# Performance work log

Hardware: AMD Instinct MI355X
Metric: run time of the kernel (lower is better)

## Reference

```python
import jax, jax.numpy as jnp
import numpy as np

DIN, HID = 256, 512
SCALE = 1.0 / (64.0 * 6.0 ** 2)  # q / 2304, as in the torch code
NEG = 9e15


def setup_inputs() -> dict:
    key = jax.random.key(0)
    ks = jax.random.split(key, 8)
    B, N = 32, 1024
    x = jax.random.normal(ks[0], (B, N, DIN), dtype=jnp.float32)
    mask = jax.random.randint(ks[1], (B, N, N), 0, 2).astype(jnp.float32)
    lim = 1.0 / np.sqrt(DIN)
    Wv = jax.random.uniform(ks[2], (DIN, HID), minval=-lim, maxval=lim, dtype=jnp.float32)
    bv = jax.random.uniform(ks[3], (HID,), minval=-lim, maxval=lim, dtype=jnp.float32)
    Wk = jax.random.uniform(ks[4], (DIN, HID), minval=-lim, maxval=lim, dtype=jnp.float32)
    bk = jax.random.uniform(ks[5], (HID,), minval=-lim, maxval=lim, dtype=jnp.float32)
    Wq = jax.random.uniform(ks[6], (DIN, HID), minval=-lim, maxval=lim, dtype=jnp.float32)
    bq = jax.random.uniform(ks[7], (HID,), minval=-lim, maxval=lim, dtype=jnp.float32)
    return {"x": x, "mask": mask, "Wv": Wv, "bv": bv, "Wk": Wk, "bk": bk, "Wq": Wq, "bq": bq}


def reference(x, mask, Wv, bv, Wk, bk, Wq, bq):
    v = jax.nn.relu(x @ Wv + bv)                      # [B,N,H]
    q = jax.nn.relu(x @ Wq + bq)                      # [B,N,H]
    k = jax.nn.relu(x @ Wk + bk)                      # [B,N,H]
    scores = jnp.einsum('bnh,bmh->bnm', q * SCALE, k)  # [B,N,N]
    att = jax.nn.softmax(scores * mask - NEG * (1.0 - mask), axis=2)
    out = jax.nn.relu(jnp.einsum('bnm,bmh->bnh', att, v))
    return out
```

## Files before the change

kernel.cpp:

```cpp
#include <hip/hip_runtime.h>
#include <hip/hip_bf16.h>

#define DIN   256
#define HID   512
#define NBAT  32
#define NSEQ  1024
#define SCALEF (1.0f / 2304.0f)
#define NEGC  9e15f

typedef __attribute__((ext_vector_type(4))) float f32x4;
typedef __attribute__((ext_vector_type(8))) short bf16x8;
typedef unsigned short u16;

__device__ __forceinline__ u16 f2bf(float f) {
    union { float f; unsigned u; } v; v.f = f;
    unsigned r = v.u + 0x7fffu + ((v.u >> 16) & 1u);
    return (u16)(r >> 16);
}

__device__ __forceinline__ float bf2f(u16 b) {
    union { unsigned u; float f; } v; v.u = ((unsigned)b) << 16;
    return v.f;
}

__device__ __forceinline__ void g2lds16(const void* g, void* l) {
    __builtin_amdgcn_global_load_lds(
        (const __attribute__((address_space(1))) void*)g,
        (__attribute__((address_space(3))) void*)l,
        16, 0, 0);
}

__global__ __launch_bounds__(256) void prep_x(const float* __restrict__ x,
                                              u16* __restrict__ xb) {
    long i = (long)blockIdx.x * 256 + threadIdx.x;
    const long n4 = (long)NBAT * NSEQ * DIN / 4;
    if (i < n4) {
        float4 v = ((const float4*)x)[i];
        ushort4 o;
        o.x = f2bf(v.x); o.y = f2bf(v.y); o.z = f2bf(v.z); o.w = f2bf(v.w);
        ((ushort4*)xb)[i] = o;
    }
}

__global__ __launch_bounds__(256) void prep_w(
    const float* __restrict__ Wv, const float* __restrict__ bv,
    const float* __restrict__ Wk, const float* __restrict__ bk,
    const float* __restrict__ Wq, const float* __restrict__ bq,
    u16* __restrict__ Wtb, float* __restrict__ biascat) {
    int i = blockIdx.x * 256 + threadIdx.x;
    if (i < 1536 * 256) {
        int n = i >> 8, k = i & 255;
        const float* W = (n < 512) ? Wv : ((n < 1024) ? Wk : Wq);
        Wtb[i] = f2bf(W[k * 512 + (n & 511)]);
    }
    if (i < 1536) {
        biascat[i] = (i < 512) ? bv[i] : ((i < 1024) ? bk[i - 512] : bq[i - 1024]);
    }
}

template<int EPI, int SWZ>
__global__ __launch_bounds__(256) void gemm_t(
    const u16* __restrict__ A, int lda, long sA,
    const u16* __restrict__ Bt, int ldb, long sB,
    void* __restrict__ Cv, int ldc, long sC,
    int K, const float* __restrict__ bias, int gx, int gy) {
    __shared__ u16 lA[128 * 64];
    __shared__ u16 lB[128 * 64];
    const int t = threadIdx.x;
    const int lane = t & 63;
    const int w = t >> 6;

    int b, bxi, byi;
    if (SWZ) {
        int f = (int)blockIdx.x;
        int per = gx * gy;
        int j = f >> 3;
        b = (f & 7) + 8 * (j / per);
        int r = j % per;
        bxi = r % gx; byi = r / gx;
    } else {
        b = blockIdx.z; bxi = blockIdx.x; byi = blockIdx.y;
    }

    const u16* Ab = A + (long)b * sA;
    const u16* Bb = Bt + (long)b * sB;
    const int bm = bxi * 128, bn = byi * 128;

    const int srow = t >> 3;
    const int csrc = ((t & 7) ^ (srow & 7)) * 8;
    const u16* gA0 = Ab + (long)(bm + srow) * lda + csrc;
    const u16* gB0 = Bb + (long)(bn + srow) * ldb + csrc;

    const int wr = (w >> 1) * 64, wc = (w & 1) * 64;
    const int frow = lane & 15;
    const int kq = lane >> 4;

    f32x4 acc[4][4] = {};

    for (int k0 = 0; k0 < K; k0 += 64) {
        __syncthreads();
#pragma unroll
        for (int p = 0; p < 4; ++p) {
            g2lds16(gA0 + (long)p * 32 * lda + k0, &lA[p * 2048 + t * 8]);
            g2lds16(gB0 + (long)p * 32 * ldb + k0, &lB[p * 2048 + t * 8]);
        }
        __syncthreads();

#pragma unroll
        for (int kk = 0; kk < 2; ++kk) {
            const int sc = ((kk * 4 + kq) ^ (frow & 7)) * 8;
            bf16x8 af[4], bfr[4];
#pragma unroll
            for (int i = 0; i < 4; ++i)
                af[i] = *(const bf16x8*)&lA[(wr + i * 16 + frow) * 64 + sc];
#pragma unroll
            for (int j = 0; j < 4; ++j)
                bfr[j] = *(const bf16x8*)&lB[(wc + j * 16 + frow) * 64 + sc];
#pragma unroll
            for (int i = 0; i < 4; ++i)
#pragma unroll
                for (int j = 0; j < 4; ++j)
                    acc[i][j] = __builtin_amdgcn_mfma_f32_16x16x32_bf16(
                        af[i], bfr[j], acc[i][j], 0, 0, 0);
        }
    }

    const int crow0 = bm + wr + (lane >> 4) * 4;
    const int ccol0 = bn + wc + (lane & 15);
#pragma unroll
    for (int i = 0; i < 4; ++i) {
#pragma unroll
        for (int j = 0; j < 4; ++j) {
            int col = ccol0 + j * 16;
#pragma unroll
            for (int r = 0; r < 4; ++r) {
                int row = crow0 + i * 16 + r;
                float v = acc[i][j][r];
                if (EPI == 0) {
                    v += bias[col];
                    v = v > 0.0f ? v : 0.0f;
                    if (col >= 1024) v *= SCALEF;
                    ((u16*)Cv)[(long)b * sC + (long)row * ldc + col] = f2bf(v);
                } else if (EPI == 1) {
                    ((u16*)Cv)[(long)b * sC + (long)row * ldc + col] = f2bf(v);
                } else {
                    ((float*)Cv)[(long)b * sC + (long)row * ldc + col] =
                        v > 0.0f ? v : 0.0f;
                }
            }
        }
    }
}

__global__ __launch_bounds__(256) void transpose_v(const u16* __restrict__ qkv,
                                                   u16* __restrict__ vt) {
    __shared__ u16 tile[64][72];
    const int t = threadIdx.x;
    const int b = blockIdx.z;
    const int n0 = blockIdx.x * 64, h0 = blockIdx.y * 64;
    const u16* src = qkv + (long)(b * NSEQ + n0) * 1536 + h0;
#pragma unroll
    for (int it = 0; it < 2; ++it) {
        int n = (t >> 3) + it * 32;
        int hc = (t & 7) * 8;
        *(bf16x8*)&tile[n][hc] = *(const bf16x8*)&src[(long)n * 1536 + hc];
    }
    __syncthreads();
    u16* dst = vt + ((long)b * HID + h0) * NSEQ + n0;
#pragma unroll
    for (int it = 0; it < 2; ++it) {
        int h = (t >> 3) + it * 32;
        int nc = (t & 7) * 8;
        bf16x8 v;
#pragma unroll
        for (int j = 0; j < 8; ++j) v[j] = (short)tile[nc + j][h];
        *(bf16x8*)&dst[(long)h * NSEQ + nc] = v;
    }
}

__global__ __launch_bounds__(256) void softmax_mask(
    u16* __restrict__ SP, const float* __restrict__ mask) {
    const long row = blockIdx.x;
    const int t = threadIdx.x;
    ushort4 sv = ((const ushort4*)(SP + row * NSEQ))[t];
    float4 mv = ((const float4*)(mask + row * NSEQ))[t];
    float l0 = mv.x * bf2f(sv.x) - NEGC * (1.0f - mv.x);
    float l1 = mv.y * bf2f(sv.y) - NEGC * (1.0f - mv.y);
    float l2 = mv.z * bf2f(sv.z) - NEGC * (1.0f - mv.z);
    float l3 = mv.w * bf2f(sv.w) - NEGC * (1.0f - mv.w);

    float mx = fmaxf(fmaxf(l0, l1), fmaxf(l2, l3));
#pragma unroll
    for (int off = 32; off; off >>= 1) mx = fmaxf(mx, __shfl_xor(mx, off));
    __shared__ float redm[4];
    if ((t & 63) == 0) redm[t >> 6] = mx;
    __syncthreads();
    mx = fmaxf(fmaxf(redm[0], redm[1]), fmaxf(redm[2], redm[3]));

    float e0 = __expf(l0 - mx), e1 = __expf(l1 - mx);
    float e2 = __expf(l2 - mx), e3 = __expf(l3 - mx);
    float sum = (e0 + e1) + (e2 + e3);
#pragma unroll
    for (int off = 32; off; off >>= 1) sum += __shfl_xor(sum, off);
    __shared__ float reds[4];
    if ((t & 63) == 0) reds[t >> 6] = sum;
    __syncthreads();
    sum = (reds[0] + reds[1]) + (reds[2] + reds[3]);

    float inv = 1.0f / sum;
    ushort4 o;
    o.x = f2bf(e0 * inv); o.y = f2bf(e1 * inv);
    o.z = f2bf(e2 * inv); o.w = f2bf(e3 * inv);
    ((ushort4*)(SP + row * NSEQ))[t] = o;
}

extern "C" void kernel_launch(void* const* d_in, const int* in_sizes, int n_in,
                              void* d_out, int out_size, void* d_ws, size_t ws_size,
                              hipStream_t stream) {
    const float* x    = (const float*)d_in[0];
    const float* mask = (const float*)d_in[1];
    const float* Wv   = (const float*)d_in[2];
    const float* bv   = (const float*)d_in[3];
    const float* Wk   = (const float*)d_in[4];
    const float* bk   = (const float*)d_in[5];
    const float* Wq   = (const float*)d_in[6];
    const float* bq   = (const float*)d_in[7];
    float* out = (float*)d_out;

    char* ws = (char*)d_ws;
    u16*   xb      = (u16*)ws;   ws += (long)NBAT * NSEQ * DIN * 2;
    u16*   Wtb     = (u16*)ws;   ws += (long)1536 * 256 * 2;
    float* biascat = (float*)ws; ws += 1536 * 4;
    u16*   qkv     = (u16*)ws;   ws += (long)NBAT * NSEQ * 1536 * 2;
    u16*   vt      = (u16*)ws;   ws += (long)NBAT * HID * NSEQ * 2;
    u16*   SP      = (u16*)ws;   ws += (long)NBAT * NSEQ * NSEQ * 2;

    prep_x<<<8192, 256, 0, stream>>>(x, xb);
    prep_w<<<1536, 256, 0, stream>>>(Wv, bv, Wk, bk, Wq, bq, Wtb, biascat);

    gemm_t<0, 0><<<dim3(256, 12, 1), 256, 0, stream>>>(
        xb, 256, 0L, Wtb, 256, 0L, qkv, 1536, 0L, 256, biascat, 0, 0);

    transpose_v<<<dim3(16, 8, NBAT), 256, 0, stream>>>(qkv, vt);

    const long sQKV = (long)NSEQ * 1536;
    gemm_t<1, 1><<<NBAT * 8 * 8, 256, 0, stream>>>(
        qkv + 1024, 1536, sQKV, qkv + 512, 1536, sQKV,
        SP, NSEQ, (long)NSEQ * NSEQ, 512, nullptr, 8, 8);

    softmax_mask<<<NBAT * NSEQ, 256, 0, stream>>>(SP, mask);

    gemm_t<2, 1><<<NBAT * 8 * 4, 256, 0, stream>>>(
        SP, NSEQ, (long)NSEQ * NSEQ, vt, NSEQ, (long)HID * NSEQ,
        out, HID, (long)NSEQ * HID, NSEQ, nullptr, 8, 4);
}
```

Baseline: 411.1 us.

## Fuse QK^T, masked softmax and PV into one attention kernel

Replaces the batched score GEMM, the row-softmax kernel and the PV GEMM with a single fused kernel. Each block takes 64 query rows, computes scores per 128-key tile, forms mask*exp(s) as bf16 probabilities in LDS, and accumulates P·V in registers, normalising by the row sums at the end. This removes the write and re-read of the full bf16 score matrix and two kernel launches. The row-max subtraction is dropped on the assumption that scaled scores are small. The price is repeated Q and V tile loads per block, only 512 blocks, and many barriers with no load/compute overlap.

```diff
diff --git a/kernel.cpp b/kernel.cpp
--- a/kernel.cpp
+++ b/kernel.cpp
@@ -6,7 +6,6 @@
 #define NBAT  32
 #define NSEQ  1024
 #define SCALEF (1.0f / 2304.0f)
-#define NEGC  9e15f
 
 typedef __attribute__((ext_vector_type(4))) float f32x4;
 typedef __attribute__((ext_vector_type(8))) short bf16x8;
@@ -58,38 +57,20 @@
     }
 }
 
-template<int EPI, int SWZ>
-__global__ __launch_bounds__(256) void gemm_t(
-    const u16* __restrict__ A, int lda, long sA,
-    const u16* __restrict__ Bt, int ldb, long sB,
-    void* __restrict__ Cv, int ldc, long sC,
-    int K, const float* __restrict__ bias, int gx, int gy) {
+__global__ __launch_bounds__(256) void gemm_qkv(
+    const u16* __restrict__ A, const u16* __restrict__ Bt,
+    u16* __restrict__ Cv, const float* __restrict__ bias) {
     __shared__ u16 lA[128 * 64];
     __shared__ u16 lB[128 * 64];
     const int t = threadIdx.x;
     const int lane = t & 63;
     const int w = t >> 6;
-
-    int b, bxi, byi;
-    if (SWZ) {
-        int f = (int)blockIdx.x;
-        int per = gx * gy;
-        int j = f >> 3;
-        b = (f & 7) + 8 * (j / per);
-        int r = j % per;
-        bxi = r % gx; byi = r / gx;
-    } else {
-        b = blockIdx.z; bxi = blockIdx.x; byi = blockIdx.y;
-    }
-
-    const u16* Ab = A + (long)b * sA;
-    const u16* Bb = Bt + (long)b * sB;
-    const int bm = bxi * 128, bn = byi * 128;
+    const int bm = blockIdx.x * 128, bn = blockIdx.y * 128;
 
     const int srow = t >> 3;
     const int csrc = ((t & 7) ^ (srow & 7)) * 8;
-    const u16* gA0 = Ab + (long)(bm + srow) * lda + csrc;
-    const u16* gB0 = Bb + (long)(bn + srow) * ldb + csrc;
+    const u16* gA0 = A + (long)(bm + srow) * 256 + csrc;
+    const u16* gB0 = Bt + (long)(bn + srow) * 256 + csrc;
 
     const int wr = (w >> 1) * 64, wc = (w & 1) * 64;
     const int frow = lane & 15;
@@ -97,15 +78,14 @@
 
     f32x4 acc[4][4] = {};
 
-    for (int k0 = 0; k0 < K; k0 += 64) {
+    for (int k0 = 0; k0 < 256; k0 += 64) {
         __syncthreads();
 #pragma unroll
         for (int p = 0; p < 4; ++p) {
-            g2lds16(gA0 + (long)p * 32 * lda + k0, &lA[p * 2048 + t * 8]);
-            g2lds16(gB0 + (long)p * 32 * ldb + k0, &lB[p * 2048 + t * 8]);
+            g2lds16(gA0 + (long)p * 32 * 256 + k0, &lA[p * 2048 + t * 8]);
+            g2lds16(gB0 + (long)p * 32 * 256 + k0, &lB[p * 2048 + t * 8]);
         }
         __syncthreads();
-
 #pragma unroll
         for (int kk = 0; kk < 2; ++kk) {
             const int sc = ((kk * 4 + kq) ^ (frow & 7)) * 8;
@@ -128,28 +108,19 @@
     const int crow0 = bm + wr + (lane >> 4) * 4;
     const int ccol0 = bn + wc + (lane & 15);
 #pragma unroll
-    for (int i = 0; i < 4; ++i) {
+    for (int i = 0; i < 4; ++i)
 #pragma unroll
         for (int j = 0; j < 4; ++j) {
             int col = ccol0 + j * 16;
 #pragma unroll
             for (int r = 0; r < 4; ++r) {
                 int row = crow0 + i * 16 + r;
-                float v = acc[i][j][r];
-                if (EPI == 0) {
-                    v += bias[col];
-                    v = v > 0.0f ? v : 0.0f;
-                    if (col >= 1024) v *= SCALEF;
-                    ((u16*)Cv)[(long)b * sC + (long)row * ldc + col] = f2bf(v);
-                } else if (EPI == 1) {
-                    ((u16*)Cv)[(long)b * sC + (long)row * ldc + col] = f2bf(v);
-                } else {
-                    ((float*)Cv)[(long)b * sC + (long)row * ldc + col] =
-                        v > 0.0f ? v : 0.0f;
-                }
-            }
-        }
-    }
+                float v = acc[i][j][r] + bias[col];
+                v = v > 0.0f ? v : 0.0f;
+                if (col >= 1024) v *= SCALEF;
+                Cv[(long)row * 1536 + col] = f2bf(v);
+            }
+        }
 }
 
 __global__ __launch_bounds__(256) void transpose_v(const u16* __restrict__ qkv,
@@ -178,40 +149,154 @@
     }
 }
 
-__global__ __launch_bounds__(256) void softmax_mask(
-    u16* __restrict__ SP, const float* __restrict__ mask) {
-    const long row = blockIdx.x;
+__global__ __launch_bounds__(256, 2) void fused_attn(
+    const u16* __restrict__ qkv, const u16* __restrict__ vt,
+    const float* __restrict__ mask, float* __restrict__ out) {
+    __shared__ u16 lQ[64 * 64];
+    __shared__ u16 lK[128 * 64];
+    __shared__ u16 lP[64 * 136];
+    __shared__ u16 lV[512 * 32];
+    __shared__ float lred[4][64];
+
     const int t = threadIdx.x;
-    ushort4 sv = ((const ushort4*)(SP + row * NSEQ))[t];
-    float4 mv = ((const float4*)(mask + row * NSEQ))[t];
-    float l0 = mv.x * bf2f(sv.x) - NEGC * (1.0f - mv.x);
-    float l1 = mv.y * bf2f(sv.y) - NEGC * (1.0f - mv.y);
-    float l2 = mv.z * bf2f(sv.z) - NEGC * (1.0f - mv.z);
-    float l3 = mv.w * bf2f(sv.w) - NEGC * (1.0f - mv.w);
-
-    float mx = fmaxf(fmaxf(l0, l1), fmaxf(l2, l3));
-#pragma unroll
-    for (int off = 32; off; off >>= 1) mx = fmaxf(mx, __shfl_xor(mx, off));
-    __shared__ float redm[4];
-    if ((t & 63) == 0) redm[t >> 6] = mx;
+    const int lane = t & 63;
+    const int w = t >> 6;
+
+    const int f = (int)blockIdx.x;
+    const int j = f >> 3;
+    const int b = (f & 7) + 8 * (j >> 4);
+    const int qt = j & 15;
+    const int n0 = qt * 64;
+
+    const u16* qb = qkv + (long)b * NSEQ * 1536 + 1024;
+    const u16* kb = qkv + (long)b * NSEQ * 1536 + 512;
+    const u16* vb = vt + (long)b * HID * NSEQ;
+    const float* mb = mask + (long)b * NSEQ * NSEQ;
+
+    const int frow = lane & 15;
+    const int kq = lane >> 4;
+
+    const int srow = t >> 3;
+    const int csrc = ((t & 7) ^ (srow & 7)) * 8;
+    const int vrow = t >> 2;
+    const int vchunk = t & 3;
+
+    f32x4 o_acc[4][8] = {};
+    float lsum[16] = {};
+
+    for (int kvt = 0; kvt < 8; ++kvt) {
+        const int kv0 = kvt * 128;
+        f32x4 s_acc[4][2] = {};
+
+        for (int d0 = 0; d0 < 512; d0 += 64) {
+            __syncthreads();
+#pragma unroll
+            for (int p = 0; p < 2; ++p)
+                g2lds16(qb + (long)(n0 + p * 32 + srow) * 1536 + d0 + csrc,
+                        &lQ[p * 2048 + t * 8]);
+#pragma unroll
+            for (int p = 0; p < 4; ++p)
+                g2lds16(kb + (long)(kv0 + p * 32 + srow) * 1536 + d0 + csrc,
+                        &lK[p * 2048 + t * 8]);
+            __syncthreads();
+#pragma unroll
+            for (int kk = 0; kk < 2; ++kk) {
+                const int sc = ((kk * 4 + kq) ^ (frow & 7)) * 8;
+                bf16x8 af[4], bf[2];
+#pragma unroll
+                for (int i = 0; i < 4; ++i)
+                    af[i] = *(const bf16x8*)&lQ[(i * 16 + frow) * 64 + sc];
+#pragma unroll
+                for (int jq = 0; jq < 2; ++jq)
+                    bf[jq] = *(const bf16x8*)&lK[(w * 32 + jq * 16 + frow) * 64 + sc];
+#pragma unroll
+                for (int i = 0; i < 4; ++i)
+#pragma unroll
+                    for (int jq = 0; jq < 2; ++jq)
+                        s_acc[i][jq] = __builtin_amdgcn_mfma_f32_16x16x32_bf16(
+                            af[i], bf[jq], s_acc[i][jq], 0, 0, 0);
+            }
+        }
+
+        __syncthreads();
+#pragma unroll
+        for (int i = 0; i < 4; ++i)
+#pragma unroll
+            for (int jq = 0; jq < 2; ++jq) {
+                const int col = w * 32 + jq * 16 + frow;
+#pragma unroll
+                for (int r = 0; r < 4; ++r) {
+                    const int row = i * 16 + (lane >> 4) * 4 + r;
+                    float mv = mb[(long)(n0 + row) * NSEQ + kv0 + col];
+                    float p = mv * __expf(s_acc[i][jq][r]);
+                    u16 pb = f2bf(p);
+                    lP[row * 136 + col] = pb;
+                    lsum[i * 4 + r] += bf2f(pb);
+                }
+            }
+
+        for (int ks = 0; ks < 4; ++ks) {
+            __syncthreads();
+#pragma unroll
+            for (int p = 0; p < 8; ++p) {
+                const int vr = p * 64 + vrow;
+                const int vc = (vchunk ^ (vr & 3)) * 8;
+                g2lds16(vb + (long)vr * NSEQ + kv0 + ks * 32 + vc,
+                        &lV[p * 2048 + t * 8]);
+            }
+            __syncthreads();
+            bf16x8 ap[4];
+#pragma unroll
+            for (int i = 0; i < 4; ++i)
+                ap[i] = *(const bf16x8*)&lP[(i * 16 + frow) * 136 + ks * 32 + kq * 8];
+#pragma unroll
+            for (int jo = 0; jo < 8; ++jo) {
+                const int h = w * 128 + jo * 16 + frow;
+                bf16x8 bv8 = *(const bf16x8*)&lV[h * 32 + ((kq ^ (h & 3)) * 8)];
+#pragma unroll
+                for (int i = 0; i < 4; ++i)
+                    o_acc[i][jo] = __builtin_amdgcn_mfma_f32_16x16x32_bf16(
+                        ap[i], bv8, o_acc[i][jo], 0, 0, 0);
+            }
+        }
+    }
+
+#pragma unroll
+    for (int s = 0; s < 16; ++s) {
+        lsum[s] += __shfl_xor(lsum[s], 1);
+        lsum[s] += __shfl_xor(lsum[s], 2);
+        lsum[s] += __shfl_xor(lsum[s], 4);
+        lsum[s] += __shfl_xor(lsum[s], 8);
+    }
+    if ((lane & 15) == 0) {
+#pragma unroll
+        for (int i = 0; i < 4; ++i)
+#pragma unroll
+            for (int r = 0; r < 4; ++r)
+                lred[w][i * 16 + (lane >> 4) * 4 + r] = lsum[i * 4 + r];
+    }
     __syncthreads();
-    mx = fmaxf(fmaxf(redm[0], redm[1]), fmaxf(redm[2], redm[3]));
-
-    float e0 = __expf(l0 - mx), e1 = __expf(l1 - mx);
-    float e2 = __expf(l2 - mx), e3 = __expf(l3 - mx);
-    float sum = (e0 + e1) + (e2 + e3);
-#pragma unroll
-    for (int off = 32; off; off >>= 1) sum += __shfl_xor(sum, off);
-    __shared__ float reds[4];
-    if ((t & 63) == 0) reds[t >> 6] = sum;
-    __syncthreads();
-    sum = (reds[0] + reds[1]) + (reds[2] + reds[3]);
-
-    float inv = 1.0f / sum;
-    ushort4 o;
-    o.x = f2bf(e0 * inv); o.y = f2bf(e1 * inv);
-    o.z = f2bf(e2 * inv); o.w = f2bf(e3 * inv);
-    ((ushort4*)(SP + row * NSEQ))[t] = o;
+    float linv[16];
+#pragma unroll
+    for (int i = 0; i < 4; ++i)
+#pragma unroll
+        for (int r = 0; r < 4; ++r) {
+            const int row = i * 16 + (lane >> 4) * 4 + r;
+            linv[i * 4 + r] = 1.0f /
+                (lred[0][row] + lred[1][row] + lred[2][row] + lred[3][row]);
+        }
+#pragma unroll
+    for (int i = 0; i < 4; ++i)
+#pragma unroll
+        for (int jo = 0; jo < 8; ++jo) {
+            const int col = w * 128 + jo * 16 + frow;
+#pragma unroll
+            for (int r = 0; r < 4; ++r) {
+                const int row = n0 + i * 16 + (lane >> 4) * 4 + r;
+                float v = o_acc[i][jo][r] * linv[i * 4 + r];
+                out[((long)b * NSEQ + row) * HID + col] = v > 0.0f ? v : 0.0f;
+            }
+        }
 }
 
 extern "C" void kernel_launch(void* const* d_in, const int* in_sizes, int n_in,
@@ -233,24 +318,13 @@
     float* biascat = (float*)ws; ws += 1536 * 4;
     u16*   qkv     = (u16*)ws;   ws += (long)NBAT * NSEQ * 1536 * 2;
     u16*   vt      = (u16*)ws;   ws += (long)NBAT * HID * NSEQ * 2;
-    u16*   SP      = (u16*)ws;   ws += (long)NBAT * NSEQ * NSEQ * 2;
 
     prep_x<<<8192, 256, 0, stream>>>(x, xb);
     prep_w<<<1536, 256, 0, stream>>>(Wv, bv, Wk, bk, Wq, bq, Wtb, biascat);
 
-    gemm_t<0, 0><<<dim3(256, 12, 1), 256, 0, stream>>>(
-        xb, 256, 0L, Wtb, 256, 0L, qkv, 1536, 0L, 256, biascat, 0, 0);
+    gemm_qkv<<<dim3(256, 12), 256, 0, stream>>>(xb, Wtb, qkv, biascat);
 
     transpose_v<<<dim3(16, 8, NBAT), 256, 0, stream>>>(qkv, vt);
 
-    const long sQKV = (long)NSEQ * 1536;
-    gemm_t<1, 1><<<NBAT * 8 * 8, 256, 0, stream>>>(
-        qkv + 1024, 1536, sQKV, qkv + 512, 1536, sQKV,
-        SP, NSEQ, (long)NSEQ * NSEQ, 512, nullptr, 8, 8);
-
-    softmax_mask<<<NBAT * NSEQ, 256, 0, stream>>>(SP, mask);
-
-    gemm_t<2, 1><<<NBAT * 8 * 4, 256, 0, stream>>>(
-        SP, NSEQ, (long)NSEQ * NSEQ, vt, NSEQ, (long)HID * NSEQ,
-        out, HID, (long)NSEQ * HID, NSEQ, nullptr, 8, 4);
-}
+    fused_attn<<<NBAT * 16, 256, 0, stream>>>(qkv, vt, mask, out);
+}
```

New measurement: 441.6 us. +7.4%, slower.
